# Performance work log

Measured on AMD Instinct MI355X. Metric: run time of the kernel, lower is better.

The kernel has to match this reference:

```python
import jax, jax.numpy as jnp
import numpy as np

B, L, M = 32768, 128, 1024  # batch, latent_size, num_basis_function


def setup_inputs() -> dict:
    key = jax.random.key(0)
    k1, k2, k3 = jax.random.split(key, 3)
    u_lat = jax.random.normal(k1, (B, L), dtype=jnp.float32)
    centres = jax.random.normal(k2, (M, L), dtype=jnp.float32)      # RBF centres (torch init: N(0,1))
    log_sigmas = jnp.zeros((M,), dtype=jnp.float32)                  # RBF log bandwidths (torch init: 0)
    lin1_w = jax.random.normal(k3, (M,), dtype=jnp.float32) / np.float32(np.sqrt(M))  # Linear(M,1,bias=False)
    return {"u_lat": u_lat, "centres": centres, "log_sigmas": log_sigmas, "lin1_w": lin1_w}


def _V_batch(u, centres, log_sigmas, lin1_w):
    """Potential V(h) = ELU(w . multiquadric(||h-c||/sigma)) + 0.5*||h||^2, per row. Returns [B]."""
    u_sq = jnp.sum(u * u, axis=-1)                                   # [B]
    c_sq = jnp.sum(centres * centres, axis=-1)                       # [M]
    # ||h - c||^2 via norm expansion: avoids [B, M, L] intermediate
    sq_dist = jnp.maximum(u_sq[:, None] + c_sq[None, :] - 2.0 * (u @ centres.T), 0.0)  # [B, M]
    d = jnp.sqrt(sq_dist) / jnp.exp(log_sigmas)[None, :]             # [B, M]
    phi = jnp.sqrt(1.0 + d * d)                                      # multiquadric kernel
    e = jax.nn.elu(phi @ lin1_w)                                     # [B]
    return e + 0.5 * u_sq


def reference(u_lat, centres, log_sigmas, lin1_w):
    # LEBNN.forward: f_lat = dV/dh evaluated per sample (vmap(jacrev) in torch).
    # Each entry of _V_batch depends only on its own row of u_lat, so
    # grad of the summed potential gives the per-sample Jacobian rows exactly.
    grad_fn = jax.grad(lambda u: jnp.sum(_V_batch(u, centres, log_sigmas, lin1_w)))
    return grad_fn(u_lat)  # [B, L]
```

## Files before the change

kernel.cpp:

```cpp
#include <hip/hip_runtime.h>
#include <math.h>

#define B_N 32768
#define L_N 128
#define M_N 1024
#define NT 512
#define TB 64
#define TM 64
#define NCHUNK (M_N / TM)

typedef __bf16 v8bf __attribute__((ext_vector_type(8)));
typedef __bf16 v4bf __attribute__((ext_vector_type(4)));
typedef float  v4f  __attribute__((ext_vector_type(4)));

#define MFMA(a, b, c) __builtin_amdgcn_mfma_f32_16x16x32_bf16(a, b, c, 0, 0, 0)

#define US  136
#define CNS 136

__device__ inline v8bf pack8(float4 a, float4 b) {
    v8bf v;
    v[0] = (__bf16)a.x; v[1] = (__bf16)a.y; v[2] = (__bf16)a.z; v[3] = (__bf16)a.w;
    v[4] = (__bf16)b.x; v[5] = (__bf16)b.y; v[6] = (__bf16)b.z; v[7] = (__bf16)b.w;
    return v;
}

__global__ void lebnn_precompute(const float* __restrict__ centres,
                                 const float* __restrict__ log_sigmas,
                                 const float* __restrict__ lin_w,
                                 float4* __restrict__ cpack) {
    int m = blockIdx.x * blockDim.x + threadIdx.x;
    if (m >= M_N) return;
    const float4* row = (const float4*)(centres + (size_t)m * L_N);
    float s = 0.f;
#pragma unroll
    for (int i = 0; i < L_N / 4; ++i) {
        float4 v = row[i];
        s += v.x * v.x + v.y * v.y + v.z * v.z + v.w * v.w;
    }
    float4 p;
    p.x = s;
    p.y = expf(-2.f * log_sigmas[m]);
    p.z = lin_w[m];
    p.w = 0.f;
    cpack[m] = p;
}

__global__ void lebnn_transpose(const float* __restrict__ centres,
                                __bf16* __restrict__ cT,
                                __bf16* __restrict__ cbn) {
    __shared__ __bf16 tile[64 * 72];
    const int m0 = blockIdx.x * 64;
    const int l0 = blockIdx.y * 64;
    const int row = threadIdx.x >> 2;
    const int seg = threadIdx.x & 3;
    const float* src = centres + (size_t)(m0 + row) * L_N + l0 + seg * 16;
    float4 a0 = *(const float4*)(src);
    float4 a1 = *(const float4*)(src + 4);
    float4 a2 = *(const float4*)(src + 8);
    float4 a3 = *(const float4*)(src + 12);
    v8bf p0 = pack8(a0, a1);
    v8bf p1 = pack8(a2, a3);
    *(v8bf*)&tile[row * 72 + seg * 16]     = p0;
    *(v8bf*)&tile[row * 72 + seg * 16 + 8] = p1;
    __bf16* rdst = cbn + (size_t)(m0 + row) * L_N + l0 + seg * 16;
    *(v8bf*)(rdst)     = p0;
    *(v8bf*)(rdst + 8) = p1;
    __syncthreads();
    v8bf o0, o1;
#pragma unroll
    for (int i = 0; i < 8; ++i) o0[i] = tile[(seg * 16 + i) * 72 + row];
#pragma unroll
    for (int i = 0; i < 8; ++i) o1[i] = tile[(seg * 16 + 8 + i) * 72 + row];
    __bf16* dst = cT + (size_t)(l0 + row) * M_N + m0 + seg * 16;
    *(v8bf*)(dst)     = o0;
    *(v8bf*)(dst + 8) = o1;
}

__global__ __launch_bounds__(NT) void lebnn_phase1(
    const float* __restrict__ u, const __bf16* __restrict__ cbn,
    const float4* __restrict__ cpack, __bf16* __restrict__ qg,
    float* __restrict__ gg, float* __restrict__ rsg)
{
    __shared__ __bf16 u_bf[64 * US];
    __shared__ float usq_s[64];
    __shared__ float upart[64 * 9];
    __shared__ float sred[288];
    __shared__ float rred[288];

    const int tid  = threadIdx.x;
    const int w    = tid >> 6;
    const int lane = tid & 63;
    const int l15  = lane & 15;
    const int l4   = lane >> 4;
    const int bh   = w >> 2;
    const int mq   = w & 3;
    const int b0   = blockIdx.x * TB;

    {
        int row = tid >> 3, seg = tid & 7;
        const float* up = u + (size_t)(b0 + row) * L_N + seg * 16;
        float4 a0 = *(const float4*)(up);
        float4 a1 = *(const float4*)(up + 4);
        float4 a2 = *(const float4*)(up + 8);
        float4 a3 = *(const float4*)(up + 12);
        float ps = a0.x*a0.x + a0.y*a0.y + a0.z*a0.z + a0.w*a0.w
                 + a1.x*a1.x + a1.y*a1.y + a1.z*a1.z + a1.w*a1.w
                 + a2.x*a2.x + a2.y*a2.y + a2.z*a2.z + a2.w*a2.w
                 + a3.x*a3.x + a3.y*a3.y + a3.z*a3.z + a3.w*a3.w;
        *(v8bf*)&u_bf[row * US + seg * 16]     = pack8(a0, a1);
        *(v8bf*)&u_bf[row * US + seg * 16 + 8] = pack8(a2, a3);
        upart[row * 9 + seg] = ps;
    }
    __syncthreads();
    if (tid < TB) {
        float s = 0.f;
#pragma unroll
        for (int i = 0; i < 8; ++i) s += upart[tid * 9 + i];
        usq_s[tid] = s;
    }
    __syncthreads();

    v8bf uf[2][4];
#pragma unroll
    for (int bt = 0; bt < 2; ++bt)
#pragma unroll
        for (int kk = 0; kk < 4; ++kk)
            uf[bt][kk] = *(v8bf*)&u_bf[(bh*32 + bt*16 + l15) * US + kk*32 + l4*8];

    float usq_r[2][4];
#pragma unroll
    for (int bt = 0; bt < 2; ++bt)
#pragma unroll
        for (int r = 0; r < 4; ++r)
            usq_r[bt][r] = usq_s[bh*32 + bt*16 + l4*4 + r];

    float s_p[2][4] = {{0.f,0.f,0.f,0.f},{0.f,0.f,0.f,0.f}};
    float r_p[2][4] = {{0.f,0.f,0.f,0.f},{0.f,0.f,0.f,0.f}};

    for (int mt = 0; mt < NCHUNK; ++mt) {
        const int m0 = mt * TM;
        float4 cpv = cpack[m0 + mq*16 + l15];
        const __bf16* bp = cbn + (size_t)(m0 + mq*16 + l15) * L_N + l4*8;

        v4f dot[2];
        dot[0] = (v4f){0.f,0.f,0.f,0.f};
        dot[1] = (v4f){0.f,0.f,0.f,0.f};
#pragma unroll
        for (int kk = 0; kk < 4; ++kk) {
            v8bf bfr = *(const v8bf*)(bp + kk*32);
            dot[0] = MFMA(uf[0][kk], bfr, dot[0]);
            dot[1] = MFMA(uf[1][kk], bfr, dot[1]);
        }

        v8bf qv8;
        const float wq = cpv.z * cpv.y;
#pragma unroll
        for (int bt = 0; bt < 2; ++bt) {
#pragma unroll
            for (int r = 0; r < 4; ++r) {
                float dv  = dot[bt][r];
                float raw = fmaf(-2.f, dv, usq_r[bt][r] + cpv.x);
                float x   = fmaf(fmaxf(raw, 0.f), cpv.y, 1.f);
                float ri  = rsqrtf(x);
                s_p[bt][r] = fmaf(cpv.z, x * ri, s_p[bt][r]);
                float qv  = (raw > 0.f) ? wq * ri : 0.f;
                r_p[bt][r] += qv;
                qv8[bt*4 + r] = (__bf16)qv;
            }
        }
        *(v8bf*)(qg + ((size_t)blockIdx.x * NCHUNK + mt) * (NT * 8) + tid * 8) = qv8;
    }

#pragma unroll
    for (int bt = 0; bt < 2; ++bt)
#pragma unroll
        for (int r = 0; r < 4; ++r) {
#pragma unroll
            for (int msk = 1; msk < 16; msk <<= 1) {
                s_p[bt][r] += __shfl_xor(s_p[bt][r], msk, 64);
                r_p[bt][r] += __shfl_xor(r_p[bt][r], msk, 64);
            }
        }
    if (l15 == 0) {
#pragma unroll
        for (int bt = 0; bt < 2; ++bt)
#pragma unroll
            for (int r = 0; r < 4; ++r) {
                sred[w*36 + bt*16 + l4*4 + r] = s_p[bt][r];
                rred[w*36 + bt*16 + l4*4 + r] = r_p[bt][r];
            }
    }
    __syncthreads();

    if (tid < TB) {
        int bhh = tid >> 5, rowr = tid & 31;
        float s = 0.f, R = 0.f;
#pragma unroll
        for (int i = 0; i < 4; ++i) {
            s += sred[(bhh*4 + i)*36 + rowr];
            R += rred[(bhh*4 + i)*36 + rowr];
        }
        float g = (s > 0.f) ? 1.f : expf(s);
        gg[b0 + tid]  = g;
        rsg[b0 + tid] = fmaf(g, R, 1.f);
    }
}

__global__ __launch_bounds__(NT) void lebnn_gemm2(
    const float* __restrict__ u, const __bf16* __restrict__ qg,
    const __bf16* __restrict__ cT, const float* __restrict__ gg,
    const float* __restrict__ rsg, float* __restrict__ out)
{
    __shared__ __bf16 qt[64 * 72];
    __shared__ __bf16 ct[128 * 72];

    const int tid  = threadIdx.x;
    const int w    = tid >> 6;
    const int lane = tid & 63;
    const int l15  = lane & 15;
    const int l4   = lane >> 4;
    const int bh   = w >> 2;
    const int lq   = w & 3;
    const int bb0  = blockIdx.x * 64;
    const int lr   = tid >> 2;
    const int sg   = tid & 3;

    v4f acc[2][2];
#pragma unroll
    for (int bt = 0; bt < 2; ++bt)
#pragma unroll
        for (int lt = 0; lt < 2; ++lt)
            acc[bt][lt] = (v4f){0.f, 0.f, 0.f, 0.f};

    v8bf qv  = *(const v8bf*)(qg + ((size_t)blockIdx.x * NCHUNK + 0) * (NT * 8) + tid * 8);
    const __bf16* csrc = cT + (size_t)lr * M_N + sg * 16;
    v8bf cva = *(const v8bf*)(csrc);
    v8bf cvb = *(const v8bf*)(csrc + 8);

    for (int mt = 0; mt < NCHUNK; ++mt) {
        __syncthreads();
        {
#pragma unroll
            for (int bt = 0; bt < 2; ++bt)
#pragma unroll
                for (int r = 0; r < 4; ++r)
                    qt[(bh*32 + bt*16 + l4*4 + r) * 72 + lq*16 + l15] = qv[bt*4 + r];
            *(v8bf*)&ct[lr * 72 + sg * 16]     = cva;
            *(v8bf*)&ct[lr * 72 + sg * 16 + 8] = cvb;
        }
        __syncthreads();

        if (mt + 1 < NCHUNK) {
            qv = *(const v8bf*)(qg + ((size_t)blockIdx.x * NCHUNK + (mt+1)) * (NT * 8) + tid * 8);
            const __bf16* cn = cT + (size_t)lr * M_N + (mt+1) * TM + sg * 16;
            cva = *(const v8bf*)(cn);
            cvb = *(const v8bf*)(cn + 8);
        }

#pragma unroll
        for (int kk = 0; kk < 2; ++kk) {
            v8bf qa0 = *(v8bf*)&qt[(bh*32 +  0 + l15) * 72 + kk*32 + l4*8];
            v8bf qa1 = *(v8bf*)&qt[(bh*32 + 16 + l15) * 72 + kk*32 + l4*8];
#pragma unroll
            for (int lt = 0; lt < 2; ++lt) {
                v8bf cb = *(v8bf*)&ct[(lq*32 + lt*16 + l15) * 72 + kk*32 + l4*8];
                acc[0][lt] = MFMA(qa0, cb, acc[0][lt]);
                acc[1][lt] = MFMA(qa1, cb, acc[1][lt]);
            }
        }
    }

    float gv[2][4], rv[2][4];
#pragma unroll
    for (int bt = 0; bt < 2; ++bt)
#pragma unroll
        for (int r = 0; r < 4; ++r) {
            int b = bb0 + bh*32 + bt*16 + l4*4 + r;
            gv[bt][r] = gg[b];
            rv[bt][r] = rsg[b];
        }
#pragma unroll
    for (int bt = 0; bt < 2; ++bt)
#pragma unroll
        for (int lt = 0; lt < 2; ++lt)
#pragma unroll
            for (int r = 0; r < 4; ++r) {
                size_t idx = (size_t)(bb0 + bh*32 + bt*16 + l4*4 + r) * L_N
                           + lq*32 + lt*16 + l15;
                out[idx] = fmaf(u[idx], rv[bt][r], -gv[bt][r] * acc[bt][lt][r]);
            }
}

#define CFS 68
#define OFF_UBF   0
#define OFF_CN    17408
#define OFF_CFL   34816
#define OFF_USQ   52224
#define OFF_UPART 52480
#define OFF_SRED  54784
#define OFF_RRED  55936
#define OFF_G     57088
#define OFF_RS    57344
#define SMEM_BYTES 57600

__global__ __launch_bounds__(NT) void lebnn_fallback(
    const float* __restrict__ u, const float* __restrict__ centres,
    const float4* __restrict__ cpack, float* __restrict__ out)
{
    extern __shared__ char smem[];
    __bf16* u_bf = (__bf16*)(smem + OFF_UBF);
    __bf16* c_n  = (__bf16*)(smem + OFF_CN);
    float*  cfl  = (float*)(smem + OFF_CFL);
    float* usq_s = (float*)(smem + OFF_USQ);
    float* upart = (float*)(smem + OFF_UPART);
    float* sred  = (float*)(smem + OFF_SRED);
    float* rred  = (float*)(smem + OFF_RRED);
    float* gsh   = (float*)(smem + OFF_G);
    float* rssh  = (float*)(smem + OFF_RS);

    const int tid  = threadIdx.x;
    const int w    = tid >> 6;
    const int lane = tid & 63;
    const int l15  = lane & 15;
    const int l4   = lane >> 4;
    const int bh   = w >> 2;
    const int mq   = w & 3;
    const int tx   = tid & 15;
    const int ty   = tid >> 4;
    const int b0   = blockIdx.x * TB;

    {
        int row = tid >> 3, seg = tid & 7;
        const float* up = u + (size_t)(b0 + row) * L_N + seg * 16;
        float4 a0 = *(const float4*)(up);
        float4 a1 = *(const float4*)(up + 4);
        float4 a2 = *(const float4*)(up + 8);
        float4 a3 = *(const float4*)(up + 12);
        float ps = a0.x*a0.x + a0.y*a0.y + a0.z*a0.z + a0.w*a0.w
                 + a1.x*a1.x + a1.y*a1.y + a1.z*a1.z + a1.w*a1.w
                 + a2.x*a2.x + a2.y*a2.y + a2.z*a2.z + a2.w*a2.w
                 + a3.x*a3.x + a3.y*a3.y + a3.z*a3.z + a3.w*a3.w;
        *(v8bf*)&u_bf[row * US + seg * 16]     = pack8(a0, a1);
        *(v8bf*)&u_bf[row * US + seg * 16 + 8] = pack8(a2, a3);
        upart[row * 9 + seg] = ps;
    }
    __syncthreads();
    if (tid < TB) {
        float s = 0.f;
#pragma unroll
        for (int i = 0; i < 8; ++i) s += upart[tid * 9 + i];
        usq_s[tid] = s;
    }
    __syncthreads();

    v8bf uf[2][4];
#pragma unroll
    for (int bt = 0; bt < 2; ++bt)
#pragma unroll
        for (int kk = 0; kk < 4; ++kk)
            uf[bt][kk] = *(v8bf*)&u_bf[(bh*32 + bt*16 + l15) * US + kk*32 + l4*8];

    float usq_r[2][4];
#pragma unroll
    for (int bt = 0; bt < 2; ++bt)
#pragma unroll
        for (int r = 0; r < 4; ++r)
            usq_r[bt][r] = usq_s[bh*32 + bt*16 + l4*4 + r];

    float s_p[2][4] = {{0.f,0.f,0.f,0.f},{0.f,0.f,0.f,0.f}};
    float r_p[2][4] = {{0.f,0.f,0.f,0.f},{0.f,0.f,0.f,0.f}};
    float T[4][4] = {{0.f}};

    const int rp = tid >> 4;
    const int cg = tid & 15;

    for (int mt = 0; mt < NCHUNK; ++mt) {
        const int m0 = mt * TM;
        __syncthreads();
        {
            const float* cp0 = centres + (size_t)(m0 + 2*rp) * L_N + cg * 8;
            float4 r0a = *(const float4*)(cp0);
            float4 r0b = *(const float4*)(cp0 + 4);
            float4 r1a = *(const float4*)(cp0 + L_N);
            float4 r1b = *(const float4*)(cp0 + L_N + 4);
            *(v8bf*)&c_n[(2*rp)     * CNS + cg*8] = pack8(r0a, r0b);
            *(v8bf*)&c_n[(2*rp + 1) * CNS + cg*8] = pack8(r1a, r1b);
        }
        float4 cpv = cpack[m0 + mq*16 + l15];
        __syncthreads();

        v4f dot[2];
        dot[0] = (v4f){0.f,0.f,0.f,0.f};
        dot[1] = (v4f){0.f,0.f,0.f,0.f};
#pragma unroll
        for (int kk = 0; kk < 4; ++kk) {
            v8bf bfr = *(v8bf*)&c_n[(mq*16 + l15) * CNS + kk*32 + l4*8];
            dot[0] = MFMA(uf[0][kk], bfr, dot[0]);
            dot[1] = MFMA(uf[1][kk], bfr, dot[1]);
        }

#pragma unroll
        for (int bt = 0; bt < 2; ++bt) {
#pragma unroll
            for (int r = 0; r < 4; ++r) {
                float dv  = dot[bt][r];
                float raw = fmaf(-2.f, dv, usq_r[bt][r] + cpv.x);
                float x   = fmaf(fmaxf(raw, 0.f), cpv.y, 1.f);
                float ri  = rsqrtf(x);
                s_p[bt][r] = fmaf(cpv.z, x * ri, s_p[bt][r]);
                float qv  = (raw > 0.f) ? cpv.z * cpv.y * ri : 0.f;
                r_p[bt][r] += qv;
                cfl[(mq*16 + l15) * CFS + bh*32 + bt*16 + l4*4 + r] = qv;
            }
        }
        __syncthreads();

        for (int mm = 0; mm < TM; ++mm) {
            v4f cf = *(v4f*)&cfl[mm * CFS + tx*4];
            v4bf cb = *(v4bf*)&c_n[mm * CNS + ty*4];
            float cv[4] = {(float)cb[0], (float)cb[1], (float)cb[2], (float)cb[3]};
#pragma unroll
            for (int i = 0; i < 4; ++i)
#pragma unroll
                for (int j = 0; j < 4; ++j)
                    T[i][j] = fmaf(cf[i], cv[j], T[i][j]);
        }
    }

    __syncthreads();

#pragma unroll
    for (int bt = 0; bt < 2; ++bt)
#pragma unroll
        for (int r = 0; r < 4; ++r) {
#pragma unroll
            for (int msk = 1; msk < 16; msk <<= 1) {
                s_p[bt][r] += __shfl_xor(s_p[bt][r], msk, 64);
                r_p[bt][r] += __shfl_xor(r_p[bt][r], msk, 64);
            }
        }
    if (l15 == 0) {
#pragma unroll
        for (int bt = 0; bt < 2; ++bt)
#pragma unroll
            for (int r = 0; r < 4; ++r) {
                sred[w*36 + bt*16 + l4*4 + r] = s_p[bt][r];
                rred[w*36 + bt*16 + l4*4 + r] = r_p[bt][r];
            }
    }
    __syncthreads();

    if (tid < TB) {
        int bhh = tid >> 5, rowr = tid & 31;
        float s = 0.f, R = 0.f;
#pragma unroll
        for (int i = 0; i < 4; ++i) {
            s += sred[(bhh*4 + i)*36 + rowr];
            R += rred[(bhh*4 + i)*36 + rowr];
        }
        float g = (s > 0.f) ? 1.f : expf(s);
        gsh[tid]  = g;
        rssh[tid] = fmaf(g, R, 1.f);
    }
    __syncthreads();

#pragma unroll
    for (int i = 0; i < 4; ++i) {
        int b = tx*4 + i;
        float rv = rssh[b];
        float gv = gsh[b];
        size_t idx = (size_t)(b0 + b) * L_N + ty*4;
        float4 uu = *(const float4*)(u + idx);
        float4 o;
        o.x = fmaf(uu.x, rv, -gv * T[i][0]);
        o.y = fmaf(uu.y, rv, -gv * T[i][1]);
        o.z = fmaf(uu.z, rv, -gv * T[i][2]);
        o.w = fmaf(uu.w, rv, -gv * T[i][3]);
        *(float4*)(out + idx) = o;
    }
}

extern "C" void kernel_launch(void* const* d_in, const int* in_sizes, int n_in,
                              void* d_out, int out_size, void* d_ws, size_t ws_size,
                              hipStream_t stream) {
    const float* u          = (const float*)d_in[0];
    const float* centres    = (const float*)d_in[1];
    const float* log_sigmas = (const float*)d_in[2];
    const float* lin_w      = (const float*)d_in[3];
    float* out = (float*)d_out;

    char* wsb = (char*)d_ws;
    float4* cpack = (float4*)wsb;
    __bf16* cT    = (__bf16*)(wsb + 16384);
    __bf16* cbn   = (__bf16*)(wsb + 278528);
    float*  gg    = (float*) (wsb + 540672);
    float*  rsg   = (float*) (wsb + 671744);
    __bf16* qg    = (__bf16*)(wsb + 802816);
    const size_t WS_NEED = 802816ULL + 67108864ULL;

    lebnn_precompute<<<(M_N + 255) / 256, 256, 0, stream>>>(centres, log_sigmas, lin_w, cpack);

    if (ws_size >= WS_NEED) {
        lebnn_transpose<<<dim3(M_N / 64, L_N / 64), 256, 0, stream>>>(centres, cT, cbn);
        lebnn_phase1<<<B_N / TB, NT, 0, stream>>>(u, cbn, cpack, qg, gg, rsg);
        lebnn_gemm2<<<B_N / 64, NT, 0, stream>>>(u, qg, cT, gg, rsg, out);
    } else {
        hipFuncSetAttribute((const void*)lebnn_fallback,
                            hipFuncAttributeMaxDynamicSharedMemorySize, SMEM_BYTES);
        lebnn_fallback<<<B_N / TB, NT, SMEM_BYTES, stream>>>(u, centres, cpack, out);
    }
}
```

Measured before the change: 75.56 us.

## Halve batch tile to 32 rows and merge setup kernels into one launch

Reduces the batch tile in phase1 and gemm2 from 64 to 32 rows, so each wave handles one 16-row MFMA tile instead of two. This doubles the grid (1024 blocks) to improve occupancy and load balance across CUs, and adds a small unroll on the phase1 loop. It also merges the precompute and transpose kernels into a single setup launch to remove a launch. The cost is that centre tiles are re-read twice as often per batch row, halving reuse in both GEMMs.

```diff
diff --git a/kernel.cpp b/kernel.cpp
--- a/kernel.cpp
+++ b/kernel.cpp
@@ -5,7 +5,7 @@
 #define L_N 128
 #define M_N 1024
 #define NT 512
-#define TB 64
+#define TB1 32
 #define TM 64
 #define NCHUNK (M_N / TM)
 
@@ -25,56 +25,58 @@
     return v;
 }
 
-__global__ void lebnn_precompute(const float* __restrict__ centres,
-                                 const float* __restrict__ log_sigmas,
-                                 const float* __restrict__ lin_w,
-                                 float4* __restrict__ cpack) {
-    int m = blockIdx.x * blockDim.x + threadIdx.x;
-    if (m >= M_N) return;
-    const float4* row = (const float4*)(centres + (size_t)m * L_N);
-    float s = 0.f;
-#pragma unroll
-    for (int i = 0; i < L_N / 4; ++i) {
-        float4 v = row[i];
-        s += v.x * v.x + v.y * v.y + v.z * v.z + v.w * v.w;
-    }
-    float4 p;
-    p.x = s;
-    p.y = expf(-2.f * log_sigmas[m]);
-    p.z = lin_w[m];
-    p.w = 0.f;
-    cpack[m] = p;
-}
-
-__global__ void lebnn_transpose(const float* __restrict__ centres,
-                                __bf16* __restrict__ cT,
-                                __bf16* __restrict__ cbn) {
+__global__ void lebnn_setup(const float* __restrict__ centres,
+                            const float* __restrict__ log_sigmas,
+                            const float* __restrict__ lin_w,
+                            float4* __restrict__ cpack,
+                            __bf16* __restrict__ cT,
+                            __bf16* __restrict__ cbn) {
     __shared__ __bf16 tile[64 * 72];
-    const int m0 = blockIdx.x * 64;
-    const int l0 = blockIdx.y * 64;
-    const int row = threadIdx.x >> 2;
-    const int seg = threadIdx.x & 3;
-    const float* src = centres + (size_t)(m0 + row) * L_N + l0 + seg * 16;
-    float4 a0 = *(const float4*)(src);
-    float4 a1 = *(const float4*)(src + 4);
-    float4 a2 = *(const float4*)(src + 8);
-    float4 a3 = *(const float4*)(src + 12);
-    v8bf p0 = pack8(a0, a1);
-    v8bf p1 = pack8(a2, a3);
-    *(v8bf*)&tile[row * 72 + seg * 16]     = p0;
-    *(v8bf*)&tile[row * 72 + seg * 16 + 8] = p1;
-    __bf16* rdst = cbn + (size_t)(m0 + row) * L_N + l0 + seg * 16;
-    *(v8bf*)(rdst)     = p0;
-    *(v8bf*)(rdst + 8) = p1;
-    __syncthreads();
-    v8bf o0, o1;
-#pragma unroll
-    for (int i = 0; i < 8; ++i) o0[i] = tile[(seg * 16 + i) * 72 + row];
-#pragma unroll
-    for (int i = 0; i < 8; ++i) o1[i] = tile[(seg * 16 + 8 + i) * 72 + row];
-    __bf16* dst = cT + (size_t)(l0 + row) * M_N + m0 + seg * 16;
-    *(v8bf*)(dst)     = o0;
-    *(v8bf*)(dst + 8) = o1;
+    const int bx = blockIdx.x;
+    if (bx < 32) {
+        const int m0 = (bx & 15) * 64;
+        const int l0 = (bx >> 4) * 64;
+        const int row = threadIdx.x >> 2;
+        const int seg = threadIdx.x & 3;
+        const float* src = centres + (size_t)(m0 + row) * L_N + l0 + seg * 16;
+        float4 a0 = *(const float4*)(src);
+        float4 a1 = *(const float4*)(src + 4);
+        float4 a2 = *(const float4*)(src + 8);
+        float4 a3 = *(const float4*)(src + 12);
+        v8bf p0 = pack8(a0, a1);
+        v8bf p1 = pack8(a2, a3);
+        *(v8bf*)&tile[row * 72 + seg * 16]     = p0;
+        *(v8bf*)&tile[row * 72 + seg * 16 + 8] = p1;
+        __bf16* rdst = cbn + (size_t)(m0 + row) * L_N + l0 + seg * 16;
+        *(v8bf*)(rdst)     = p0;
+        *(v8bf*)(rdst + 8) = p1;
+        __syncthreads();
+        v8bf o0, o1;
+#pragma unroll
+        for (int i = 0; i < 8; ++i) o0[i] = tile[(seg * 16 + i) * 72 + row];
+#pragma unroll
+        for (int i = 0; i < 8; ++i) o1[i] = tile[(seg * 16 + 8 + i) * 72 + row];
+        __bf16* dst = cT + (size_t)(l0 + row) * M_N + m0 + seg * 16;
+        *(v8bf*)(dst)     = o0;
+        *(v8bf*)(dst + 8) = o1;
+    } else {
+        int m = (bx - 32) * 256 + threadIdx.x;
+        if (m < M_N) {
+            const float4* row = (const float4*)(centres + (size_t)m * L_N);
+            float s = 0.f;
+#pragma unroll
+            for (int i = 0; i < L_N / 4; ++i) {
+                float4 v = row[i];
+                s += v.x * v.x + v.y * v.y + v.z * v.z + v.w * v.w;
+            }
+            float4 p;
+            p.x = s;
+            p.y = expf(-2.f * log_sigmas[m]);
+            p.z = lin_w[m];
+            p.w = 0.f;
+            cpack[m] = p;
+        }
+    }
 }
 
 __global__ __launch_bounds__(NT) void lebnn_phase1(
@@ -82,11 +84,11 @@
     const float4* __restrict__ cpack, __bf16* __restrict__ qg,
     float* __restrict__ gg, float* __restrict__ rsg)
 {
-    __shared__ __bf16 u_bf[64 * US];
-    __shared__ float usq_s[64];
-    __shared__ float upart[64 * 9];
-    __shared__ float sred[288];
-    __shared__ float rred[288];
+    __shared__ __bf16 u_bf[TB1 * US];
+    __shared__ float usq_s[TB1];
+    __shared__ float upart[TB1 * 17];
+    __shared__ float sred[8 * 20];
+    __shared__ float rred[8 * 20];
 
     const int tid  = threadIdx.x;
     const int w    = tid >> 6;
@@ -95,7 +97,210 @@
     const int l4   = lane >> 4;
     const int bh   = w >> 2;
     const int mq   = w & 3;
-    const int b0   = blockIdx.x * TB;
+    const int b0   = blockIdx.x * TB1;
+
+    {
+        int row = tid >> 4;
+        int seg = tid & 15;
+        const float* up = u + (size_t)(b0 + row) * L_N + seg * 8;
+        float4 a0 = *(const float4*)(up);
+        float4 a1 = *(const float4*)(up + 4);
+        float ps = a0.x*a0.x + a0.y*a0.y + a0.z*a0.z + a0.w*a0.w
+                 + a1.x*a1.x + a1.y*a1.y + a1.z*a1.z + a1.w*a1.w;
+        *(v8bf*)&u_bf[row * US + seg * 8] = pack8(a0, a1);
+        upart[row * 17 + seg] = ps;
+    }
+    __syncthreads();
+    if (tid < TB1) {
+        float s = 0.f;
+#pragma unroll
+        for (int i = 0; i < 16; ++i) s += upart[tid * 17 + i];
+        usq_s[tid] = s;
+    }
+    __syncthreads();
+
+    v8bf uf[4];
+#pragma unroll
+    for (int kk = 0; kk < 4; ++kk)
+        uf[kk] = *(v8bf*)&u_bf[(bh*16 + l15) * US + kk*32 + l4*8];
+
+    float usq_r[4];
+#pragma unroll
+    for (int r = 0; r < 4; ++r)
+        usq_r[r] = usq_s[bh*16 + l4*4 + r];
+
+    float s_p[4] = {0.f, 0.f, 0.f, 0.f};
+    float r_p[4] = {0.f, 0.f, 0.f, 0.f};
+
+#pragma unroll 2
+    for (int mt = 0; mt < NCHUNK; ++mt) {
+        const int m0 = mt * TM;
+        float4 cpv = cpack[m0 + mq*16 + l15];
+        const __bf16* bp = cbn + (size_t)(m0 + mq*16 + l15) * L_N + l4*8;
+
+        v4f dot = (v4f){0.f, 0.f, 0.f, 0.f};
+#pragma unroll
+        for (int kk = 0; kk < 4; ++kk)
+            dot = MFMA(uf[kk], *(const v8bf*)(bp + kk*32), dot);
+
+        v4bf qv4;
+        const float wq = cpv.z * cpv.y;
+#pragma unroll
+        for (int r = 0; r < 4; ++r) {
+            float dv  = dot[r];
+            float raw = fmaf(-2.f, dv, usq_r[r] + cpv.x);
+            float x   = fmaf(fmaxf(raw, 0.f), cpv.y, 1.f);
+            float ri  = rsqrtf(x);
+            s_p[r] = fmaf(cpv.z, x * ri, s_p[r]);
+            float qv  = (raw > 0.f) ? wq * ri : 0.f;
+            r_p[r] += qv;
+            qv4[r] = (__bf16)qv;
+        }
+        *(v4bf*)(qg + ((size_t)blockIdx.x * NCHUNK + mt) * (NT * 4) + tid * 4) = qv4;
+    }
+
+#pragma unroll
+    for (int r = 0; r < 4; ++r) {
+#pragma unroll
+        for (int msk = 1; msk < 16; msk <<= 1) {
+            s_p[r] += __shfl_xor(s_p[r], msk, 64);
+            r_p[r] += __shfl_xor(r_p[r], msk, 64);
+        }
+    }
+    if (l15 == 0) {
+#pragma unroll
+        for (int r = 0; r < 4; ++r) {
+            sred[w*20 + l4*4 + r] = s_p[r];
+            rred[w*20 + l4*4 + r] = r_p[r];
+        }
+    }
+    __syncthreads();
+
+    if (tid < TB1) {
+        int bh2 = tid >> 4, rowr = tid & 15;
+        float s = 0.f, R = 0.f;
+#pragma unroll
+        for (int i = 0; i < 4; ++i) {
+            s += sred[(bh2*4 + i)*20 + rowr];
+            R += rred[(bh2*4 + i)*20 + rowr];
+        }
+        float g = (s > 0.f) ? 1.f : expf(s);
+        gg[b0 + tid]  = g;
+        rsg[b0 + tid] = fmaf(g, R, 1.f);
+    }
+}
+
+__global__ __launch_bounds__(NT) void lebnn_gemm2(
+    const float* __restrict__ u, const __bf16* __restrict__ qg,
+    const __bf16* __restrict__ cT, const float* __restrict__ gg,
+    const float* __restrict__ rsg, float* __restrict__ out)
+{
+    __shared__ __bf16 qt[TB1 * 72];
+    __shared__ __bf16 ct[128 * 72];
+
+    const int tid  = threadIdx.x;
+    const int w    = tid >> 6;
+    const int lane = tid & 63;
+    const int l15  = lane & 15;
+    const int l4   = lane >> 4;
+    const int bh   = w >> 2;
+    const int lq   = w & 3;
+    const int bb0  = blockIdx.x * TB1;
+    const int lr   = tid >> 2;
+    const int sg   = tid & 3;
+
+    v4f acc[2];
+    acc[0] = (v4f){0.f, 0.f, 0.f, 0.f};
+    acc[1] = (v4f){0.f, 0.f, 0.f, 0.f};
+
+    v4bf qv = *(const v4bf*)(qg + ((size_t)blockIdx.x * NCHUNK + 0) * (NT * 4) + tid * 4);
+    const __bf16* csrc = cT + (size_t)lr * M_N + sg * 16;
+    v8bf cva = *(const v8bf*)(csrc);
+    v8bf cvb = *(const v8bf*)(csrc + 8);
+
+    for (int mt = 0; mt < NCHUNK; ++mt) {
+        __syncthreads();
+        {
+#pragma unroll
+            for (int r = 0; r < 4; ++r)
+                qt[(bh*16 + l4*4 + r) * 72 + lq*16 + l15] = qv[r];
+            *(v8bf*)&ct[lr * 72 + sg * 16]     = cva;
+            *(v8bf*)&ct[lr * 72 + sg * 16 + 8] = cvb;
+        }
+        __syncthreads();
+
+        if (mt + 1 < NCHUNK) {
+            qv = *(const v4bf*)(qg + ((size_t)blockIdx.x * NCHUNK + (mt+1)) * (NT * 4) + tid * 4);
+            const __bf16* cn = cT + (size_t)lr * M_N + (mt+1) * TM + sg * 16;
+            cva = *(const v8bf*)(cn);
+            cvb = *(const v8bf*)(cn + 8);
+        }
+
+#pragma unroll
+        for (int kk = 0; kk < 2; ++kk) {
+            v8bf qa = *(v8bf*)&qt[(bh*16 + l15) * 72 + kk*32 + l4*8];
+#pragma unroll
+            for (int lt = 0; lt < 2; ++lt) {
+                v8bf cb = *(v8bf*)&ct[(lq*32 + lt*16 + l15) * 72 + kk*32 + l4*8];
+                acc[lt] = MFMA(qa, cb, acc[lt]);
+            }
+        }
+    }
+
+    float gv[4], rv[4];
+#pragma unroll
+    for (int r = 0; r < 4; ++r) {
+        int b = bb0 + bh*16 + l4*4 + r;
+        gv[r] = gg[b];
+        rv[r] = rsg[b];
+    }
+#pragma unroll
+    for (int lt = 0; lt < 2; ++lt)
+#pragma unroll
+        for (int r = 0; r < 4; ++r) {
+            size_t idx = (size_t)(bb0 + bh*16 + l4*4 + r) * L_N
+                       + lq*32 + lt*16 + l15;
+            out[idx] = fmaf(u[idx], rv[r], -gv[r] * acc[lt][r]);
+        }
+}
+
+#define CFS 68
+#define OFF_UBF   0
+#define OFF_CN    17408
+#define OFF_CFL   34816
+#define OFF_USQ   52224
+#define OFF_UPART 52480
+#define OFF_SRED  54784
+#define OFF_RRED  55936
+#define OFF_G     57088
+#define OFF_RS    57344
+#define SMEM_BYTES 57600
+
+__global__ __launch_bounds__(NT) void lebnn_fallback(
+    const float* __restrict__ u, const float* __restrict__ centres,
+    const float4* __restrict__ cpack, float* __restrict__ out)
+{
+    extern __shared__ char smem[];
+    __bf16* u_bf = (__bf16*)(smem + OFF_UBF);
+    __bf16* c_n  = (__bf16*)(smem + OFF_CN);
+    float*  cfl  = (float*)(smem + OFF_CFL);
+    float* usq_s = (float*)(smem + OFF_USQ);
+    float* upart = (float*)(smem + OFF_UPART);
+    float* sred  = (float*)(smem + OFF_SRED);
+    float* rred  = (float*)(smem + OFF_RRED);
+    float* gsh   = (float*)(smem + OFF_G);
+    float* rssh  = (float*)(smem + OFF_RS);
+
+    const int tid  = threadIdx.x;
+    const int w    = tid >> 6;
+    const int lane = tid & 63;
+    const int l15  = lane & 15;
+    const int l4   = lane >> 4;
+    const int bh   = w >> 2;
+    const int mq   = w & 3;
+    const int tx   = tid & 15;
+    const int ty   = tid >> 4;
+    const int b0   = blockIdx.x * 64;
 
     {
         int row = tid >> 3, seg = tid & 7;
@@ -113,240 +318,7 @@
         upart[row * 9 + seg] = ps;
     }
     __syncthreads();
-    if (tid < TB) {
-        float s = 0.f;
-#pragma unroll
-        for (int i = 0; i < 8; ++i) s += upart[tid * 9 + i];
-        usq_s[tid] = s;
-    }
-    __syncthreads();
-
-    v8bf uf[2][4];
-#pragma unroll
-    for (int bt = 0; bt < 2; ++bt)
-#pragma unroll
-        for (int kk = 0; kk < 4; ++kk)
-            uf[bt][kk] = *(v8bf*)&u_bf[(bh*32 + bt*16 + l15) * US + kk*32 + l4*8];
-
-    float usq_r[2][4];
-#pragma unroll
-    for (int bt = 0; bt < 2; ++bt)
-#pragma unroll
-        for (int r = 0; r < 4; ++r)
-            usq_r[bt][r] = usq_s[bh*32 + bt*16 + l4*4 + r];
-
-    float s_p[2][4] = {{0.f,0.f,0.f,0.f},{0.f,0.f,0.f,0.f}};
-    float r_p[2][4] = {{0.f,0.f,0.f,0.f},{0.f,0.f,0.f,0.f}};
-
-    for (int mt = 0; mt < NCHUNK; ++mt) {
-        const int m0 = mt * TM;
-        float4 cpv = cpack[m0 + mq*16 + l15];
-        const __bf16* bp = cbn + (size_t)(m0 + mq*16 + l15) * L_N + l4*8;
-
-        v4f dot[2];
-        dot[0] = (v4f){0.f,0.f,0.f,0.f};
-        dot[1] = (v4f){0.f,0.f,0.f,0.f};
-#pragma unroll
-        for (int kk = 0; kk < 4; ++kk) {
-            v8bf bfr = *(const v8bf*)(bp + kk*32);
-            dot[0] = MFMA(uf[0][kk], bfr, dot[0]);
-            dot[1] = MFMA(uf[1][kk], bfr, dot[1]);
-        }
-
-        v8bf qv8;
-        const float wq = cpv.z * cpv.y;
-#pragma unroll
-        for (int bt = 0; bt < 2; ++bt) {
-#pragma unroll
-            for (int r = 0; r < 4; ++r) {
-                float dv  = dot[bt][r];
-                float raw = fmaf(-2.f, dv, usq_r[bt][r] + cpv.x);
-                float x   = fmaf(fmaxf(raw, 0.f), cpv.y, 1.f);
-                float ri  = rsqrtf(x);
-                s_p[bt][r] = fmaf(cpv.z, x * ri, s_p[bt][r]);
-                float qv  = (raw > 0.f) ? wq * ri : 0.f;
-                r_p[bt][r] += qv;
-                qv8[bt*4 + r] = (__bf16)qv;
-            }
-        }
-        *(v8bf*)(qg + ((size_t)blockIdx.x * NCHUNK + mt) * (NT * 8) + tid * 8) = qv8;
-    }
-
-#pragma unroll
-    for (int bt = 0; bt < 2; ++bt)
-#pragma unroll
-        for (int r = 0; r < 4; ++r) {
-#pragma unroll
-            for (int msk = 1; msk < 16; msk <<= 1) {
-                s_p[bt][r] += __shfl_xor(s_p[bt][r], msk, 64);
-                r_p[bt][r] += __shfl_xor(r_p[bt][r], msk, 64);
-            }
-        }
-    if (l15 == 0) {
-#pragma unroll
-        for (int bt = 0; bt < 2; ++bt)
-#pragma unroll
-            for (int r = 0; r < 4; ++r) {
-                sred[w*36 + bt*16 + l4*4 + r] = s_p[bt][r];
-                rred[w*36 + bt*16 + l4*4 + r] = r_p[bt][r];
-            }
-    }
-    __syncthreads();
-
-    if (tid < TB) {
-        int bhh = tid >> 5, rowr = tid & 31;
-        float s = 0.f, R = 0.f;
-#pragma unroll
-        for (int i = 0; i < 4; ++i) {
-            s += sred[(bhh*4 + i)*36 + rowr];
-            R += rred[(bhh*4 + i)*36 + rowr];
-        }
-        float g = (s > 0.f) ? 1.f : expf(s);
-        gg[b0 + tid]  = g;
-        rsg[b0 + tid] = fmaf(g, R, 1.f);
-    }
-}
-
-__global__ __launch_bounds__(NT) void lebnn_gemm2(
-    const float* __restrict__ u, const __bf16* __restrict__ qg,
-    const __bf16* __restrict__ cT, const float* __restrict__ gg,
-    const float* __restrict__ rsg, float* __restrict__ out)
-{
-    __shared__ __bf16 qt[64 * 72];
-    __shared__ __bf16 ct[128 * 72];
-
-    const int tid  = threadIdx.x;
-    const int w    = tid >> 6;
-    const int lane = tid & 63;
-    const int l15  = lane & 15;
-    const int l4   = lane >> 4;
-    const int bh   = w >> 2;
-    const int lq   = w & 3;
-    const int bb0  = blockIdx.x * 64;
-    const int lr   = tid >> 2;
-    const int sg   = tid & 3;
-
-    v4f acc[2][2];
-#pragma unroll
-    for (int bt = 0; bt < 2; ++bt)
-#pragma unroll
-        for (int lt = 0; lt < 2; ++lt)
-            acc[bt][lt] = (v4f){0.f, 0.f, 0.f, 0.f};
-
-    v8bf qv  = *(const v8bf*)(qg + ((size_t)blockIdx.x * NCHUNK + 0) * (NT * 8) + tid * 8);
-    const __bf16* csrc = cT + (size_t)lr * M_N + sg * 16;
-    v8bf cva = *(const v8bf*)(csrc);
-    v8bf cvb = *(const v8bf*)(csrc + 8);
-
-    for (int mt = 0; mt < NCHUNK; ++mt) {
-        __syncthreads();
-        {
-#pragma unroll
-            for (int bt = 0; bt < 2; ++bt)
-#pragma unroll
-                for (int r = 0; r < 4; ++r)
-                    qt[(bh*32 + bt*16 + l4*4 + r) * 72 + lq*16 + l15] = qv[bt*4 + r];
-            *(v8bf*)&ct[lr * 72 + sg * 16]     = cva;
-            *(v8bf*)&ct[lr * 72 + sg * 16 + 8] = cvb;
-        }
-        __syncthreads();
-
-        if (mt + 1 < NCHUNK) {
-            qv = *(const v8bf*)(qg + ((size_t)blockIdx.x * NCHUNK + (mt+1)) * (NT * 8) + tid * 8);
-            const __bf16* cn = cT + (size_t)lr * M_N + (mt+1) * TM + sg * 16;
-            cva = *(const v8bf*)(cn);
-            cvb = *(const v8bf*)(cn + 8);
-        }
-
-#pragma unroll
-        for (int kk = 0; kk < 2; ++kk) {
-            v8bf qa0 = *(v8bf*)&qt[(bh*32 +  0 + l15) * 72 + kk*32 + l4*8];
-            v8bf qa1 = *(v8bf*)&qt[(bh*32 + 16 + l15) * 72 + kk*32 + l4*8];
-#pragma unroll
-            for (int lt = 0; lt < 2; ++lt) {
-                v8bf cb = *(v8bf*)&ct[(lq*32 + lt*16 + l15) * 72 + kk*32 + l4*8];
-                acc[0][lt] = MFMA(qa0, cb, acc[0][lt]);
-                acc[1][lt] = MFMA(qa1, cb, acc[1][lt]);
-            }
-        }
-    }
-
-    float gv[2][4], rv[2][4];
-#pragma unroll
-    for (int bt = 0; bt < 2; ++bt)
-#pragma unroll
-        for (int r = 0; r < 4; ++r) {
-            int b = bb0 + bh*32 + bt*16 + l4*4 + r;
-            gv[bt][r] = gg[b];
-            rv[bt][r] = rsg[b];
-        }
-#pragma unroll
-    for (int bt = 0; bt < 2; ++bt)
-#pragma unroll
-        for (int lt = 0; lt < 2; ++lt)
-#pragma unroll
-            for (int r = 0; r < 4; ++r) {
-                size_t idx = (size_t)(bb0 + bh*32 + bt*16 + l4*4 + r) * L_N
-                           + lq*32 + lt*16 + l15;
-                out[idx] = fmaf(u[idx], rv[bt][r], -gv[bt][r] * acc[bt][lt][r]);
-            }
-}
-
-#define CFS 68
-#define OFF_UBF   0
-#define OFF_CN    17408
-#define OFF_CFL   34816
-#define OFF_USQ   52224
-#define OFF_UPART 52480
-#define OFF_SRED  54784
-#define OFF_RRED  55936
-#define OFF_G     57088
-#define OFF_RS    57344
-#define SMEM_BYTES 57600
-
-__global__ __launch_bounds__(NT) void lebnn_fallback(
-    const float* __restrict__ u, const float* __restrict__ centres,
-    const float4* __restrict__ cpack, float* __restrict__ out)
-{
-    extern __shared__ char smem[];
-    __bf16* u_bf = (__bf16*)(smem + OFF_UBF);
-    __bf16* c_n  = (__bf16*)(smem + OFF_CN);
-    float*  cfl  = (float*)(smem + OFF_CFL);
-    float* usq_s = (float*)(smem + OFF_USQ);
-    float* upart = (float*)(smem + OFF_UPART);
-    float* sred  = (float*)(smem + OFF_SRED);
-    float* rred  = (float*)(smem + OFF_RRED);
-    float* gsh   = (float*)(smem + OFF_G);
-    float* rssh  = (float*)(smem + OFF_RS);
-
-    const int tid  = threadIdx.x;
-    const int w    = tid >> 6;
-    const int lane = tid & 63;
-    const int l15  = lane & 15;
-    const int l4   = lane >> 4;
-    const int bh   = w >> 2;
-    const int mq   = w & 3;
-    const int tx   = tid & 15;
-    const int ty   = tid >> 4;
-    const int b0   = blockIdx.x * TB;
-
-    {
-        int row = tid >> 3, seg = tid & 7;
-        const float* up = u + (size_t)(b0 + row) * L_N + seg * 16;
-        float4 a0 = *(const float4*)(up);
-        float4 a1 = *(const float4*)(up + 4);
-        float4 a2 = *(const float4*)(up + 8);
-        float4 a3 = *(const float4*)(up + 12);
-        float ps = a0.x*a0.x + a0.y*a0.y + a0.z*a0.z + a0.w*a0.w
-                 + a1.x*a1.x + a1.y*a1.y + a1.z*a1.z + a1.w*a1.w
-                 + a2.x*a2.x + a2.y*a2.y + a2.z*a2.z + a2.w*a2.w
-                 + a3.x*a3.x + a3.y*a3.y + a3.z*a3.z + a3.w*a3.w;
-        *(v8bf*)&u_bf[row * US + seg * 16]     = pack8(a0, a1);
-        *(v8bf*)&u_bf[row * US + seg * 16 + 8] = pack8(a2, a3);
-        upart[row * 9 + seg] = ps;
-    }
-    __syncthreads();
-    if (tid < TB) {
+    if (tid < 64) {
         float s = 0.f;
 #pragma unroll
         for (int i = 0; i < 8; ++i) s += upart[tid * 9 + i];
@@ -451,7 +423,7 @@
     }
     __syncthreads();
 
-    if (tid < TB) {
+    if (tid < 64) {
         int bhh = tid >> 5, rowr = tid & 31;
         float s = 0.f, R = 0.f;
 #pragma unroll
@@ -499,15 +471,14 @@
     __bf16* qg    = (__bf16*)(wsb + 802816);
     const size_t WS_NEED = 802816ULL + 67108864ULL;
 
-    lebnn_precompute<<<(M_N + 255) / 256, 256, 0, stream>>>(centres, log_sigmas, lin_w, cpack);
-
     if (ws_size >= WS_NEED) {
-        lebnn_transpose<<<dim3(M_N / 64, L_N / 64), 256, 0, stream>>>(centres, cT, cbn);
-        lebnn_phase1<<<B_N / TB, NT, 0, stream>>>(u, cbn, cpack, qg, gg, rsg);
-        lebnn_gemm2<<<B_N / 64, NT, 0, stream>>>(u, qg, cT, gg, rsg, out);
+        lebnn_setup<<<36, 256, 0, stream>>>(centres, log_sigmas, lin_w, cpack, cT, cbn);
+        lebnn_phase1<<<B_N / TB1, NT, 0, stream>>>(u, cbn, cpack, qg, gg, rsg);
+        lebnn_gemm2<<<B_N / TB1, NT, 0, stream>>>(u, qg, cT, gg, rsg, out);
     } else {
+        lebnn_setup<<<36, 256, 0, stream>>>(centres, log_sigmas, lin_w, cpack, cT, cbn);
         hipFuncSetAttribute((const void*)lebnn_fallback,
                             hipFuncAttributeMaxDynamicSharedMemorySize, SMEM_BYTES);
-        lebnn_fallback<<<B_N / TB, NT, SMEM_BYTES, stream>>>(u, centres, cpack, out);
-    }
-}
+        lebnn_fallback<<<B_N / 64, NT, SMEM_BYTES, stream>>>(u, centres, cpack, out);
+    }
+}
```

After: 103.9 us. 1.38x slower.

## Store intermediate q matrix as scaled fp8, stage centres in LDS, merge setup kernels

Applied to the files above, without the earlier changes.

The B×M intermediate q written by phase1 and read by gemm2 is now quantised to fp8 with a fixed scale of 64 instead of bf16. This halves that round-trip through global memory, and the scale is undone in the gemm2 epilogue and in the rsg term. Phase1 also stages each 64-row centre chunk into shared memory with block barriers instead of reading fragments straight from global memory. The precompute and transpose kernels are merged into a single launch. The fp8 storage lowers gradient precision and can underflow or saturate outside the scaled range, and the extra barriers in phase1 may add stalls.

```diff
diff --git a/kernel.cpp b/kernel.cpp
--- a/kernel.cpp
+++ b/kernel.cpp
@@ -12,11 +12,15 @@
 typedef __bf16 v8bf __attribute__((ext_vector_type(8)));
 typedef __bf16 v4bf __attribute__((ext_vector_type(4)));
 typedef float  v4f  __attribute__((ext_vector_type(4)));
+typedef float  v2f  __attribute__((ext_vector_type(2)));
+typedef unsigned int u32x2 __attribute__((ext_vector_type(2)));
 
 #define MFMA(a, b, c) __builtin_amdgcn_mfma_f32_16x16x32_bf16(a, b, c, 0, 0, 0)
 
 #define US  136
 #define CNS 136
+#define QSCALE 64.0f
+#define QINV   0.015625f
 
 __device__ inline v8bf pack8(float4 a, float4 b) {
     v8bf v;
@@ -25,66 +29,69 @@
     return v;
 }
 
-__global__ void lebnn_precompute(const float* __restrict__ centres,
-                                 const float* __restrict__ log_sigmas,
-                                 const float* __restrict__ lin_w,
-                                 float4* __restrict__ cpack) {
-    int m = blockIdx.x * blockDim.x + threadIdx.x;
-    if (m >= M_N) return;
-    const float4* row = (const float4*)(centres + (size_t)m * L_N);
-    float s = 0.f;
-#pragma unroll
-    for (int i = 0; i < L_N / 4; ++i) {
-        float4 v = row[i];
-        s += v.x * v.x + v.y * v.y + v.z * v.z + v.w * v.w;
-    }
-    float4 p;
-    p.x = s;
-    p.y = expf(-2.f * log_sigmas[m]);
-    p.z = lin_w[m];
-    p.w = 0.f;
-    cpack[m] = p;
-}
-
-__global__ void lebnn_transpose(const float* __restrict__ centres,
-                                __bf16* __restrict__ cT,
-                                __bf16* __restrict__ cbn) {
+__global__ void lebnn_setup(const float* __restrict__ centres,
+                            const float* __restrict__ log_sigmas,
+                            const float* __restrict__ lin_w,
+                            float4* __restrict__ cpack,
+                            __bf16* __restrict__ cT,
+                            __bf16* __restrict__ cbn) {
     __shared__ __bf16 tile[64 * 72];
-    const int m0 = blockIdx.x * 64;
-    const int l0 = blockIdx.y * 64;
-    const int row = threadIdx.x >> 2;
-    const int seg = threadIdx.x & 3;
-    const float* src = centres + (size_t)(m0 + row) * L_N + l0 + seg * 16;
-    float4 a0 = *(const float4*)(src);
-    float4 a1 = *(const float4*)(src + 4);
-    float4 a2 = *(const float4*)(src + 8);
-    float4 a3 = *(const float4*)(src + 12);
-    v8bf p0 = pack8(a0, a1);
-    v8bf p1 = pack8(a2, a3);
-    *(v8bf*)&tile[row * 72 + seg * 16]     = p0;
-    *(v8bf*)&tile[row * 72 + seg * 16 + 8] = p1;
-    __bf16* rdst = cbn + (size_t)(m0 + row) * L_N + l0 + seg * 16;
-    *(v8bf*)(rdst)     = p0;
-    *(v8bf*)(rdst + 8) = p1;
-    __syncthreads();
-    v8bf o0, o1;
-#pragma unroll
-    for (int i = 0; i < 8; ++i) o0[i] = tile[(seg * 16 + i) * 72 + row];
-#pragma unroll
-    for (int i = 0; i < 8; ++i) o1[i] = tile[(seg * 16 + 8 + i) * 72 + row];
-    __bf16* dst = cT + (size_t)(l0 + row) * M_N + m0 + seg * 16;
-    *(v8bf*)(dst)     = o0;
-    *(v8bf*)(dst + 8) = o1;
+    const int bx = blockIdx.x;
+    if (bx < 32) {
+        const int m0 = (bx & 15) * 64;
+        const int l0 = (bx >> 4) * 64;
+        const int row = threadIdx.x >> 2;
+        const int seg = threadIdx.x & 3;
+        const float* src = centres + (size_t)(m0 + row) * L_N + l0 + seg * 16;
+        float4 a0 = *(const float4*)(src);
+        float4 a1 = *(const float4*)(src + 4);
+        float4 a2 = *(const float4*)(src + 8);
+        float4 a3 = *(const float4*)(src + 12);
+        v8bf p0 = pack8(a0, a1);
+        v8bf p1 = pack8(a2, a3);
+        *(v8bf*)&tile[row * 72 + seg * 16]     = p0;
+        *(v8bf*)&tile[row * 72 + seg * 16 + 8] = p1;
+        __bf16* rdst = cbn + (size_t)(m0 + row) * L_N + l0 + seg * 16;
+        *(v8bf*)(rdst)     = p0;
+        *(v8bf*)(rdst + 8) = p1;
+        __syncthreads();
+        v8bf o0, o1;
+#pragma unroll
+        for (int i = 0; i < 8; ++i) o0[i] = tile[(seg * 16 + i) * 72 + row];
+#pragma unroll
+        for (int i = 0; i < 8; ++i) o1[i] = tile[(seg * 16 + 8 + i) * 72 + row];
+        __bf16* dst = cT + (size_t)(l0 + row) * M_N + m0 + seg * 16;
+        *(v8bf*)(dst)     = o0;
+        *(v8bf*)(dst + 8) = o1;
+    } else {
+        int m = (bx - 32) * 256 + threadIdx.x;
+        if (m < M_N) {
+            const float4* row = (const float4*)(centres + (size_t)m * L_N);
+            float s = 0.f;
+#pragma unroll
+            for (int i = 0; i < L_N / 4; ++i) {
+                float4 v = row[i];
+                s += v.x * v.x + v.y * v.y + v.z * v.z + v.w * v.w;
+            }
+            float4 p;
+            p.x = s;
+            p.y = expf(-2.f * log_sigmas[m]);
+            p.z = lin_w[m];
+            p.w = 0.f;
+            cpack[m] = p;
+        }
+    }
 }
 
 __global__ __launch_bounds__(NT) void lebnn_phase1(
     const float* __restrict__ u, const __bf16* __restrict__ cbn,
-    const float4* __restrict__ cpack, __bf16* __restrict__ qg,
+    const float4* __restrict__ cpack, unsigned int* __restrict__ qg32,
     float* __restrict__ gg, float* __restrict__ rsg)
 {
-    __shared__ __bf16 u_bf[64 * US];
-    __shared__ float usq_s[64];
-    __shared__ float upart[64 * 9];
+    __shared__ __bf16 u_bf[TB * US];
+    __shared__ __bf16 c_n[TM * CNS];
+    __shared__ float usq_s[TB];
+    __shared__ float upart[TB * 9];
     __shared__ float sred[288];
     __shared__ float rred[288];
 
@@ -138,23 +145,32 @@
     float s_p[2][4] = {{0.f,0.f,0.f,0.f},{0.f,0.f,0.f,0.f}};
     float r_p[2][4] = {{0.f,0.f,0.f,0.f},{0.f,0.f,0.f,0.f}};
 
+    const int srow = tid >> 3;
+    const int sseg = tid & 7;
+
     for (int mt = 0; mt < NCHUNK; ++mt) {
         const int m0 = mt * TM;
+        __syncthreads();
+        {
+            const __bf16* cp = cbn + (size_t)(m0 + srow) * L_N + sseg * 16;
+            *(v8bf*)&c_n[srow * CNS + sseg * 16]     = *(const v8bf*)(cp);
+            *(v8bf*)&c_n[srow * CNS + sseg * 16 + 8] = *(const v8bf*)(cp + 8);
+        }
         float4 cpv = cpack[m0 + mq*16 + l15];
-        const __bf16* bp = cbn + (size_t)(m0 + mq*16 + l15) * L_N + l4*8;
+        __syncthreads();
 
         v4f dot[2];
         dot[0] = (v4f){0.f,0.f,0.f,0.f};
         dot[1] = (v4f){0.f,0.f,0.f,0.f};
 #pragma unroll
         for (int kk = 0; kk < 4; ++kk) {
-            v8bf bfr = *(const v8bf*)(bp + kk*32);
+            v8bf bfr = *(v8bf*)&c_n[(mq*16 + l15) * CNS + kk*32 + l4*8];
             dot[0] = MFMA(uf[0][kk], bfr, dot[0]);
             dot[1] = MFMA(uf[1][kk], bfr, dot[1]);
         }
 
-        v8bf qv8;
-        const float wq = cpv.z * cpv.y;
+        float qs[8];
+        const float wqs = cpv.z * cpv.y * QSCALE;
 #pragma unroll
         for (int bt = 0; bt < 2; ++bt) {
 #pragma unroll
@@ -164,12 +180,18 @@
                 float x   = fmaf(fmaxf(raw, 0.f), cpv.y, 1.f);
                 float ri  = rsqrtf(x);
                 s_p[bt][r] = fmaf(cpv.z, x * ri, s_p[bt][r]);
-                float qv  = (raw > 0.f) ? wq * ri : 0.f;
+                float qv  = (raw > 0.f) ? wqs * ri : 0.f;
                 r_p[bt][r] += qv;
-                qv8[bt*4 + r] = (__bf16)qv;
-            }
-        }
-        *(v8bf*)(qg + ((size_t)blockIdx.x * NCHUNK + mt) * (NT * 8) + tid * 8) = qv8;
+                qs[bt*4 + r] = qv;
+            }
+        }
+        unsigned int w0 = 0, w1 = 0;
+        w0 = __builtin_amdgcn_cvt_pk_fp8_f32(qs[0], qs[1], w0, false);
+        w0 = __builtin_amdgcn_cvt_pk_fp8_f32(qs[2], qs[3], w0, true);
+        w1 = __builtin_amdgcn_cvt_pk_fp8_f32(qs[4], qs[5], w1, false);
+        w1 = __builtin_amdgcn_cvt_pk_fp8_f32(qs[6], qs[7], w1, true);
+        u32x2 qw; qw[0] = w0; qw[1] = w1;
+        *(u32x2*)(qg32 + ((size_t)blockIdx.x * NCHUNK + mt) * (NT * 2) + tid * 2) = qw;
     }
 
 #pragma unroll
@@ -203,12 +225,12 @@
         }
         float g = (s > 0.f) ? 1.f : expf(s);
         gg[b0 + tid]  = g;
-        rsg[b0 + tid] = fmaf(g, R, 1.f);
+        rsg[b0 + tid] = fmaf(g * QINV, R, 1.f);
     }
 }
 
 __global__ __launch_bounds__(NT) void lebnn_gemm2(
-    const float* __restrict__ u, const __bf16* __restrict__ qg,
+    const float* __restrict__ u, const unsigned int* __restrict__ qg32,
     const __bf16* __restrict__ cT, const float* __restrict__ gg,
     const float* __restrict__ rsg, float* __restrict__ out)
 {
@@ -233,7 +255,7 @@
         for (int lt = 0; lt < 2; ++lt)
             acc[bt][lt] = (v4f){0.f, 0.f, 0.f, 0.f};
 
-    v8bf qv  = *(const v8bf*)(qg + ((size_t)blockIdx.x * NCHUNK + 0) * (NT * 8) + tid * 8);
+    u32x2 qw = *(const u32x2*)(qg32 + ((size_t)blockIdx.x * NCHUNK + 0) * (NT * 2) + tid * 2);
     const __bf16* csrc = cT + (size_t)lr * M_N + sg * 16;
     v8bf cva = *(const v8bf*)(csrc);
     v8bf cvb = *(const v8bf*)(csrc + 8);
@@ -241,18 +263,27 @@
     for (int mt = 0; mt < NCHUNK; ++mt) {
         __syncthreads();
         {
+            v2f p0 = __builtin_amdgcn_cvt_pk_f32_fp8(qw[0], false);
+            v2f p1 = __builtin_amdgcn_cvt_pk_f32_fp8(qw[0], true);
+            v2f p2 = __builtin_amdgcn_cvt_pk_f32_fp8(qw[1], false);
+            v2f p3 = __builtin_amdgcn_cvt_pk_f32_fp8(qw[1], true);
+            __bf16 qb[8];
+            qb[0] = (__bf16)p0[0]; qb[1] = (__bf16)p0[1];
+            qb[2] = (__bf16)p1[0]; qb[3] = (__bf16)p1[1];
+            qb[4] = (__bf16)p2[0]; qb[5] = (__bf16)p2[1];
+            qb[6] = (__bf16)p3[0]; qb[7] = (__bf16)p3[1];
 #pragma unroll
             for (int bt = 0; bt < 2; ++bt)
 #pragma unroll
                 for (int r = 0; r < 4; ++r)
-                    qt[(bh*32 + bt*16 + l4*4 + r) * 72 + lq*16 + l15] = qv[bt*4 + r];
+                    qt[(bh*32 + bt*16 + l4*4 + r) * 72 + lq*16 + l15] = qb[bt*4 + r];
             *(v8bf*)&ct[lr * 72 + sg * 16]     = cva;
             *(v8bf*)&ct[lr * 72 + sg * 16 + 8] = cvb;
         }
         __syncthreads();
 
         if (mt + 1 < NCHUNK) {
-            qv = *(const v8bf*)(qg + ((size_t)blockIdx.x * NCHUNK + (mt+1)) * (NT * 8) + tid * 8);
+            qw = *(const u32x2*)(qg32 + ((size_t)blockIdx.x * NCHUNK + (mt+1)) * (NT * 2) + tid * 2);
             const __bf16* cn = cT + (size_t)lr * M_N + (mt+1) * TM + sg * 16;
             cva = *(const v8bf*)(cn);
             cvb = *(const v8bf*)(cn + 8);
@@ -277,7 +308,7 @@
 #pragma unroll
         for (int r = 0; r < 4; ++r) {
             int b = bb0 + bh*32 + bt*16 + l4*4 + r;
-            gv[bt][r] = gg[b];
+            gv[bt][r] = gg[b] * QINV;
             rv[bt][r] = rsg[b];
         }
 #pragma unroll
@@ -328,7 +359,7 @@
     const int mq   = w & 3;
     const int tx   = tid & 15;
     const int ty   = tid >> 4;
-    const int b0   = blockIdx.x * TB;
+    const int b0   = blockIdx.x * 64;
 
     {
         int row = tid >> 3, seg = tid & 7;
@@ -346,7 +377,7 @@
         upart[row * 9 + seg] = ps;
     }
     __syncthreads();
-    if (tid < TB) {
+    if (tid < 64) {
         float s = 0.f;
 #pragma unroll
         for (int i = 0; i < 8; ++i) s += upart[tid * 9 + i];
@@ -451,7 +482,7 @@
     }
     __syncthreads();
 
-    if (tid < TB) {
+    if (tid < 64) {
         int bhh = tid >> 5, rowr = tid & 31;
         float s = 0.f, R = 0.f;
 #pragma unroll
@@ -496,18 +527,17 @@
     __bf16* cbn   = (__bf16*)(wsb + 278528);
     float*  gg    = (float*) (wsb + 540672);
     float*  rsg   = (float*) (wsb + 671744);
-    __bf16* qg    = (__bf16*)(wsb + 802816);
-    const size_t WS_NEED = 802816ULL + 67108864ULL;
-
-    lebnn_precompute<<<(M_N + 255) / 256, 256, 0, stream>>>(centres, log_sigmas, lin_w, cpack);
+    unsigned int* qg32 = (unsigned int*)(wsb + 802816);
+    const size_t WS_NEED = 802816ULL + 33554432ULL;
+
+    lebnn_setup<<<36, 256, 0, stream>>>(centres, log_sigmas, lin_w, cpack, cT, cbn);
 
     if (ws_size >= WS_NEED) {
-        lebnn_transpose<<<dim3(M_N / 64, L_N / 64), 256, 0, stream>>>(centres, cT, cbn);
-        lebnn_phase1<<<B_N / TB, NT, 0, stream>>>(u, cbn, cpack, qg, gg, rsg);
-        lebnn_gemm2<<<B_N / 64, NT, 0, stream>>>(u, qg, cT, gg, rsg, out);
+        lebnn_phase1<<<B_N / TB, NT, 0, stream>>>(u, cbn, cpack, qg32, gg, rsg);
+        lebnn_gemm2<<<B_N / 64, NT, 0, stream>>>(u, qg32, cT, gg, rsg, out);
     } else {
         hipFuncSetAttribute((const void*)lebnn_fallback,
                             hipFuncAttributeMaxDynamicSharedMemorySize, SMEM_BYTES);
-        lebnn_fallback<<<B_N / TB, NT, SMEM_BYTES, stream>>>(u, centres, cpack, out);
+        lebnn_fallback<<<B_N / 64, NT, SMEM_BYTES, stream>>>(u, centres, cpack, out);
     }
 }
```

After: 63.35 us. 16.2% less time.
